# Kernel optimization log

Measured on AMD Instinct MI355X. Metric: run time of the kernel, lower is better.

## Reference

```python
import jax, jax.numpy as jnp
import numpy as np
import math

B, IN_CH, OUT_CH, STYLE, KS, DIL, L = 16, 128, 256, 512, 3, 1, 16384


def setup_inputs() -> dict:
    key = jax.random.key(0)
    ks = jax.random.split(key, 6)
    return {
        "x": jax.random.normal(ks[0], (B, IN_CH, L), jnp.float32),
        "style": jax.random.normal(ks[1], (B, STYLE), jnp.float32),
        "conv_weight": jax.random.normal(ks[2], (1, OUT_CH, IN_CH, KS), jnp.float32),
        "mod_weight": jax.random.normal(ks[3], (IN_CH, STYLE), jnp.float32),
        "mod_bias": jnp.ones((IN_CH,), jnp.float32),  # bias_init=1 in EqualLinear
        "out_v": jax.random.normal(ks[4], (IN_CH, OUT_CH // 2, 1), jnp.float32),
        "out_g": jax.random.uniform(ks[5], (IN_CH, 1, 1), jnp.float32, 0.5, 1.5),
        "out_bias": jnp.zeros((IN_CH,), jnp.float32),
    }


def reference(x, style, conv_weight, mod_weight, mod_bias, out_v, out_g, out_bias):
    scale_conv = 1.0 / math.sqrt(IN_CH * KS ** 2)  # fan_in = in_channel * k**2
    scale_mod = 1.0 / math.sqrt(STYLE)             # EqualLinear scale, lr_mul=1

    # modulation: EqualLinear(style_dim -> in_channel)
    s = style @ (mod_weight * scale_mod).T + mod_bias            # [B, I]

    # per-sample modulated + demodulated conv weight
    w = scale_conv * conv_weight * s[:, None, :, None]           # [B, O, I, K]
    demod = jax.lax.rsqrt(jnp.sum(w * w, axis=(2, 3)) + 1e-8)    # [B, O]
    w = w * demod[:, :, None, None]

    # grouped (groups=batch) dilated conv1d == per-sample conv via unfold + einsum
    pad = (KS - 1) // 2 * DIL
    xp = jnp.pad(x, ((0, 0), (0, 0), (pad, pad)))
    patches = jnp.stack([xp[:, :, k * DIL:k * DIL + L] for k in range(KS)], axis=2)  # [B, I, K, L]
    out = jnp.einsum('boik,bikl->bol', w, patches)               # [B, O, L]

    # gated tanh-sigmoid
    xa, xb = jnp.split(out, 2, axis=1)
    g = jnp.tanh(xa) * jax.nn.sigmoid(xb)                        # [B, O//2, L]

    # weight-normed 1x1 conv (dim=0: norm over in_ch and k per out channel)
    vnorm = jnp.sqrt(jnp.sum(out_v * out_v, axis=(1, 2), keepdims=True))
    w1 = (out_g * out_v / vnorm)[:, :, 0]                        # [R, O//2]
    y = jnp.einsum('oc,bcl->bol', w1, g) + out_bias[None, :, None]

    return (y + x) * math.sqrt(0.5)
```

## Files before the change

### kernel.cpp

```cpp
#include <hip/hip_runtime.h>
#include <hip/hip_bf16.h>
#include <math.h>

typedef float f32x4 __attribute__((ext_vector_type(4)));
typedef short bh8  __attribute__((ext_vector_type(8)));
typedef unsigned int u32x4 __attribute__((ext_vector_type(4)));

#define B_   16
#define IC   128
#define OC   256
#define RC   128
#define STY  512
#define KS_  3
#define LL   16384
#define LT   128

#define WS_S_OFF   0
#define WS_W_OFF   8192
#define WS_W1_OFF  (8192 + 3145728)

#define SMEM_BYTES 33792

__device__ __forceinline__ unsigned short f2b(float f) {
    union { float f; unsigned int u; } z; z.f = f;
    unsigned int u = z.u;
    return (unsigned short)((u + 0x7fffu + ((u >> 16) & 1u)) >> 16);
}

__device__ __forceinline__ float b2f(unsigned int u16) {
    union { unsigned int u; float f; } z; z.u = u16 << 16;
    return z.f;
}

__device__ __forceinline__ unsigned int pack2bf(float a, float b) {
    __hip_bfloat162 p = __float22bfloat162_rn(make_float2(a, b));
    return *(unsigned int*)&p;
}

__global__ void k_style(const float* __restrict__ style, const float* __restrict__ mw,
                        const float* __restrict__ mb, float* __restrict__ s_out) {
    const int b = blockIdx.x, i = threadIdx.x;
    const float4* st = (const float4*)(style + b * STY);
    const float4* w  = (const float4*)(mw + (size_t)i * STY);
    float acc = 0.f;
#pragma unroll 4
    for (int j = 0; j < STY / 4; ++j) {
        float4 a = st[j], c = w[j];
        acc += a.x * c.x + a.y * c.y + a.z * c.z + a.w * c.w;
    }
    s_out[b * IC + i] = acc * 0.044194173824159216f + mb[i];
}

__global__ void k_modw(const float* __restrict__ cw, const float* __restrict__ s,
                       unsigned short* __restrict__ wbf) {
    const int o = blockIdx.x, b = blockIdx.y, i = threadIdx.x;
    const float sv = s[b * IC + i] * 0.029462782549439476f;
    const float w0 = cw[(o * IC + i) * KS_ + 0] * sv;
    const float w1 = cw[(o * IC + i) * KS_ + 1] * sv;
    const float w2 = cw[(o * IC + i) * KS_ + 2] * sv;
    float ss = w0 * w0 + w1 * w1 + w2 * w2;
    for (int off = 32; off; off >>= 1) ss += __shfl_down(ss, off, 64);
    __shared__ float red[2];
    if ((i & 63) == 0) red[i >> 6] = ss;
    __syncthreads();
    const float d = rsqrtf(red[0] + red[1] + 1e-8f);
    unsigned short* dst = wbf + ((size_t)b * OC + o) * 384 + i;
    dst[0]   = f2b(w0 * d);
    dst[128] = f2b(w1 * d);
    dst[256] = f2b(w2 * d);
}

__global__ void k_w1(const float* __restrict__ v, const float* __restrict__ g,
                     unsigned short* __restrict__ w1bf) {
    const int o = blockIdx.x, c = threadIdx.x;
    const float vv = v[o * RC + c];
    float ss = vv * vv;
    for (int off = 32; off; off >>= 1) ss += __shfl_down(ss, off, 64);
    __shared__ float red[2];
    if ((c & 63) == 0) red[c >> 6] = ss;
    __syncthreads();
    w1bf[o * RC + c] = f2b(g[o] * vv * rsqrtf(red[0] + red[1]));
}

__global__ __launch_bounds__(512, 4) void k_main(
    const float* __restrict__ x, const unsigned short* __restrict__ wbf,
    const unsigned short* __restrict__ w1bf, const float* __restrict__ obias,
    float* __restrict__ out) {
    __shared__ alignas(16) char smem[SMEM_BYTES];

    const int t = threadIdx.x;
    const int lane = t & 63, wv = t >> 6;
    const int lm = lane & 15, kg = lane >> 4;
    const int c0 = wv * 16 + kg * 4;

    const int lid = blockIdx.y * (LL / LT) + blockIdx.x;
    const int swz = (lid & 7) * 256 + (lid >> 3);
    const int b  = swz >> 7;
    const int l0 = (swz & 127) * LT;

    const float* xb = x + (size_t)b * IC * LL + l0;

    {
        const int chb = wv * 16;
#pragma unroll
        for (int p = 0; p < 2; ++p) {
            const int pos = lane + p * 64;
            const int row = pos + 1;
#pragma unroll
            for (int h = 0; h < 2; ++h) {
                float xv[8];
#pragma unroll
                for (int c = 0; c < 8; ++c)
                    xv[c] = xb[(size_t)(chb + h * 8 + c) * LL + pos];
                u32x4 wvec;
                wvec.x = pack2bf(xv[0], xv[1]);
                wvec.y = pack2bf(xv[2], xv[3]);
                wvec.z = pack2bf(xv[4], xv[5]);
                wvec.w = pack2bf(xv[6], xv[7]);
                *(u32x4*)(smem + row * 256 +
                          (((chb + h * 8) * 2) ^ ((row & 15) << 4))) = wvec;
            }
        }
    }
    if (t < 128) {
        const float* hx = x + ((size_t)b * IC + t) * LL;
        float lf = (l0 > 0) ? hx[l0 - 1] : 0.f;
        float rt = (l0 + LT < LL) ? hx[l0 + LT] : 0.f;
        *(unsigned short*)(smem + 0 * 256 + ((t * 2) ^ ((0 & 15) << 4)))   = f2b(lf);
        *(unsigned short*)(smem + 129 * 256 + ((t * 2) ^ ((129 & 15) << 4))) = f2b(rt);
    }
    __syncthreads();

    f32x4 acc[2][8];
#pragma unroll
    for (int m = 0; m < 2; ++m)
#pragma unroll
        for (int nt = 0; nt < 8; ++nt) acc[m][nt] = (f32x4){0.f, 0.f, 0.f, 0.f};

    const unsigned short* wa = wbf + ((size_t)b * OC + wv * 16 + lm) * 384 + kg * 8;
    const unsigned short* wb2 = wa + 128 * 384;

    bh8 ca0 = *(const bh8*)(wa + 0);
    bh8 ca1 = *(const bh8*)(wb2 + 0);
#pragma unroll
    for (int kc = 0; kc < 12; ++kc) {
        bh8 na0 = ca0, na1 = ca1;
        if (kc < 11) {
            const int nkoff = ((kc + 1) >> 2) * 128 + ((kc + 1) & 3) * 32;
            na0 = *(const bh8*)(wa + nkoff);
            na1 = *(const bh8*)(wb2 + nkoff);
        }
        const int tap = kc >> 2;
        const int icb = (kc & 3) * 32;
#pragma unroll
        for (int nt = 0; nt < 8; ++nt) {
            const int lr = nt * 16 + lm + tap;
            const bh8 bf = *(const bh8*)(smem + lr * 256 +
                                         (((icb + kg * 8) * 2) ^ ((lr & 15) << 4)));
            acc[0][nt] = __builtin_amdgcn_mfma_f32_16x16x32_bf16(ca0, bf, acc[0][nt], 0, 0, 0);
            acc[1][nt] = __builtin_amdgcn_mfma_f32_16x16x32_bf16(ca1, bf, acc[1][nt], 0, 0, 0);
        }
        ca0 = na0; ca1 = na1;
    }

    unsigned long long xr[8];
#pragma unroll
    for (int nt = 0; nt < 8; ++nt) {
        const int row = nt * 16 + lm + 1;
        xr[nt] = *(const unsigned long long*)(smem + row * 256 +
                                             ((c0 * 2) ^ ((row & 15) << 4)));
    }

    const unsigned short* w1p = w1bf + (wv * 16 + lm) * RC + kg * 8;
    bh8 w1f[4];
#pragma unroll
    for (int kc = 0; kc < 4; ++kc) w1f[kc] = *(const bh8*)(w1p + kc * 32);

    unsigned long long gw[8];
#pragma unroll
    for (int nt = 0; nt < 8; ++nt) {
        float g4[4];
#pragma unroll
        for (int j = 0; j < 4; ++j) {
            const float xa = acc[0][nt][j], xg = acc[1][nt][j];
            const float th = 1.f - 2.f * __builtin_amdgcn_rcpf(__expf(2.f * xa) + 1.f);
            const float sg = __builtin_amdgcn_rcpf(1.f + __expf(-xg));
            g4[j] = th * sg;
        }
        gw[nt] = (unsigned long long)pack2bf(g4[0], g4[1]) |
                 ((unsigned long long)pack2bf(g4[2], g4[3]) << 32);
    }
    __syncthreads();

#pragma unroll
    for (int nt = 0; nt < 8; ++nt) {
        const int n = nt * 16 + lm;
        *(unsigned long long*)(smem + n * 256 + ((c0 * 2) ^ ((n & 15) << 4))) = gw[nt];
    }
    __syncthreads();

    f32x4 acc2[8];
#pragma unroll
    for (int nt = 0; nt < 8; ++nt) acc2[nt] = (f32x4){0.f, 0.f, 0.f, 0.f};
#pragma unroll
    for (int kc = 0; kc < 4; ++kc) {
#pragma unroll
        for (int nt = 0; nt < 8; ++nt) {
            const int n = nt * 16 + lm;
            const bh8 bf = *(const bh8*)(smem + n * 256 +
                                         (((kc * 32 + kg * 8) * 2) ^ ((n & 15) << 4)));
            acc2[nt] = __builtin_amdgcn_mfma_f32_16x16x32_bf16(w1f[kc], bf, acc2[nt], 0, 0, 0);
        }
    }
    __syncthreads();

    const float4 bias4 = *(const float4*)(obias + c0);
    const float bias[4] = {bias4.x, bias4.y, bias4.z, bias4.w};
#pragma unroll
    for (int nt = 0; nt < 8; ++nt) {
        const int n = nt * 16 + lm;
        float o4[4];
#pragma unroll
        for (int j = 0; j < 4; ++j)
            o4[j] = (acc2[nt][j] + bias[j] + b2f((unsigned int)(xr[nt] >> (16 * j)) & 0xffffu))
                    * 0.70710678118654752f;
        *(unsigned long long*)(smem + n * 264 + c0 * 2) =
            (unsigned long long)pack2bf(o4[0], o4[1]) |
            ((unsigned long long)pack2bf(o4[2], o4[3]) << 32);
    }
    __syncthreads();

    {
        const int p4 = t & 31;
        const int cb = t >> 5;
        float* ob = out + (size_t)b * IC * LL + l0 + p4 * 4;
#pragma unroll
        for (int h = 0; h < 2; ++h) {
            const int chb = cb * 4 + h * 64;
            unsigned long long yq[4];
#pragma unroll
            for (int q = 0; q < 4; ++q)
                yq[q] = *(const unsigned long long*)(smem + (p4 * 4 + q) * 264 + chb * 2);
#pragma unroll
            for (int e = 0; e < 4; ++e) {
                float4 ov;
                ov.x = b2f((unsigned int)(yq[0] >> (16 * e)) & 0xffffu);
                ov.y = b2f((unsigned int)(yq[1] >> (16 * e)) & 0xffffu);
                ov.z = b2f((unsigned int)(yq[2] >> (16 * e)) & 0xffffu);
                ov.w = b2f((unsigned int)(yq[3] >> (16 * e)) & 0xffffu);
                *(float4*)(ob + (size_t)(chb + e) * LL) = ov;
            }
        }
    }
}

extern "C" void kernel_launch(void* const* d_in, const int* in_sizes, int n_in,
                              void* d_out, int out_size, void* d_ws, size_t ws_size,
                              hipStream_t stream) {
    (void)in_sizes; (void)n_in; (void)out_size; (void)ws_size;
    const float* x        = (const float*)d_in[0];
    const float* style    = (const float*)d_in[1];
    const float* conv_w   = (const float*)d_in[2];
    const float* mod_w    = (const float*)d_in[3];
    const float* mod_b    = (const float*)d_in[4];
    const float* out_v    = (const float*)d_in[5];
    const float* out_g    = (const float*)d_in[6];
    const float* out_bias = (const float*)d_in[7];
    float* out = (float*)d_out;

    float* s_buf = (float*)((char*)d_ws + WS_S_OFF);
    unsigned short* wbf  = (unsigned short*)((char*)d_ws + WS_W_OFF);
    unsigned short* w1bf = (unsigned short*)((char*)d_ws + WS_W1_OFF);

    k_style<<<dim3(B_), 128, 0, stream>>>(style, mod_w, mod_b, s_buf);
    k_modw<<<dim3(OC, B_), 128, 0, stream>>>(conv_w, s_buf, wbf);
    k_w1<<<dim3(RC), 128, 0, stream>>>(out_v, out_g, w1bf);
    k_main<<<dim3(LL / LT, B_), 512, 0, stream>>>(x, wbf, w1bf, out_bias, out);
}
```

Measured before the change: 143.0 us.

## Process two L-tiles per block with register prefetch of the next x tile

Each block now handles two consecutive 128-position tiles. The x data for the second tile is loaded into registers while the first tile's conv and gate stages run, which hides global load latency. The grid is halved to a 1D launch with an XCD-aware batch mapping. This adds 32+ registers per thread, which could reduce occupancy under the 512x4 launch bounds or cause spills.

New measurement: 306.7 us. 2.14x slower.

```diff
diff --git a/kernel.cpp b/kernel.cpp
--- a/kernel.cpp
+++ b/kernel.cpp
@@ -14,6 +14,7 @@
 #define KS_  3
 #define LL   16384
 #define LT   128
+#define NT_  2
 
 #define WS_S_OFF   0
 #define WS_W_OFF   8192
@@ -93,162 +94,223 @@
     const int lm = lane & 15, kg = lane >> 4;
     const int c0 = wv * 16 + kg * 4;
 
-    const int lid = blockIdx.y * (LL / LT) + blockIdx.x;
-    const int swz = (lid & 7) * 256 + (lid >> 3);
-    const int b  = swz >> 7;
-    const int l0 = (swz & 127) * LT;
-
-    const float* xb = x + (size_t)b * IC * LL + l0;
-
-    {
-        const int chb = wv * 16;
-#pragma unroll
-        for (int p = 0; p < 2; ++p) {
-            const int pos = lane + p * 64;
-            const int row = pos + 1;
-#pragma unroll
-            for (int h = 0; h < 2; ++h) {
-                float xv[8];
+    const int lid = blockIdx.x;
+    const int xcd = lid & 7, idx = lid >> 3;
+    const int b   = xcd * 2 + (idx >> 6);
+    const int l0b = (idx & 63) * (LT * NT_);
+
+    const float* xbase = x + (size_t)b * IC * LL;
+    const unsigned short* wa  = wbf + ((size_t)b * OC + wv * 16 + lm) * 384 + kg * 8;
+    const unsigned short* wb2 = wa + 128 * 384;
+    const unsigned short* w1p = w1bf + (wv * 16 + lm) * RC + kg * 8;
+
+    float pf0[16], pf1[16];
+    float pfh0 = 0.f, pfh1 = 0.f;
+
+#pragma unroll
+    for (int tt = 0; tt < NT_; ++tt) {
+        const int l0 = l0b + tt * LT;
+        const float* xb = xbase + l0;
+
+        if (tt == 1) __syncthreads();
+
+        if (tt == 0) {
+            const int chb = wv * 16;
+#pragma unroll
+            for (int p = 0; p < 2; ++p) {
+                const int pos = lane + p * 64;
+                const int row = pos + 1;
+#pragma unroll
+                for (int h = 0; h < 2; ++h) {
+                    float xv[8];
+#pragma unroll
+                    for (int c = 0; c < 8; ++c)
+                        xv[c] = xb[(size_t)(chb + h * 8 + c) * LL + pos];
+                    u32x4 wvec;
+                    wvec.x = pack2bf(xv[0], xv[1]);
+                    wvec.y = pack2bf(xv[2], xv[3]);
+                    wvec.z = pack2bf(xv[4], xv[5]);
+                    wvec.w = pack2bf(xv[6], xv[7]);
+                    *(u32x4*)(smem + row * 256 +
+                              (((chb + h * 8) * 2) ^ ((row & 15) << 4))) = wvec;
+                }
+            }
+            if (t < 128) {
+                const float* hx = xbase + (size_t)t * LL;
+                float lf = (l0 > 0) ? hx[l0 - 1] : 0.f;
+                float rt = (l0 + LT < LL) ? hx[l0 + LT] : 0.f;
+                *(unsigned short*)(smem + 0 * 256 + ((t * 2) ^ ((0 & 15) << 4)))     = f2b(lf);
+                *(unsigned short*)(smem + 129 * 256 + ((t * 2) ^ ((129 & 15) << 4))) = f2b(rt);
+            }
+        } else {
+            const int chb = wv * 16;
+#pragma unroll
+            for (int p = 0; p < 2; ++p) {
+                const int row = lane + p * 64 + 1;
+#pragma unroll
+                for (int h = 0; h < 2; ++h) {
+                    u32x4 wvec;
+                    if (h == 0) {
+                        wvec.x = pack2bf(pf0[p * 8 + 0], pf0[p * 8 + 1]);
+                        wvec.y = pack2bf(pf0[p * 8 + 2], pf0[p * 8 + 3]);
+                        wvec.z = pack2bf(pf0[p * 8 + 4], pf0[p * 8 + 5]);
+                        wvec.w = pack2bf(pf0[p * 8 + 6], pf0[p * 8 + 7]);
+                    } else {
+                        wvec.x = pack2bf(pf1[p * 8 + 0], pf1[p * 8 + 1]);
+                        wvec.y = pack2bf(pf1[p * 8 + 2], pf1[p * 8 + 3]);
+                        wvec.z = pack2bf(pf1[p * 8 + 4], pf1[p * 8 + 5]);
+                        wvec.w = pack2bf(pf1[p * 8 + 6], pf1[p * 8 + 7]);
+                    }
+                    *(u32x4*)(smem + row * 256 +
+                              (((chb + h * 8) * 2) ^ ((row & 15) << 4))) = wvec;
+                }
+            }
+            if (t < 128) {
+                *(unsigned short*)(smem + 0 * 256 + ((t * 2) ^ ((0 & 15) << 4)))     = f2b(pfh0);
+                *(unsigned short*)(smem + 129 * 256 + ((t * 2) ^ ((129 & 15) << 4))) = f2b(pfh1);
+            }
+        }
+        __syncthreads();
+
+        if (tt == 0) {
+            const float* xb1 = xbase + l0b + LT;
+#pragma unroll
+            for (int p = 0; p < 2; ++p)
 #pragma unroll
                 for (int c = 0; c < 8; ++c)
-                    xv[c] = xb[(size_t)(chb + h * 8 + c) * LL + pos];
-                u32x4 wvec;
-                wvec.x = pack2bf(xv[0], xv[1]);
-                wvec.y = pack2bf(xv[2], xv[3]);
-                wvec.z = pack2bf(xv[4], xv[5]);
-                wvec.w = pack2bf(xv[6], xv[7]);
-                *(u32x4*)(smem + row * 256 +
-                          (((chb + h * 8) * 2) ^ ((row & 15) << 4))) = wvec;
-            }
-        }
-    }
-    if (t < 128) {
-        const float* hx = x + ((size_t)b * IC + t) * LL;
-        float lf = (l0 > 0) ? hx[l0 - 1] : 0.f;
-        float rt = (l0 + LT < LL) ? hx[l0 + LT] : 0.f;
-        *(unsigned short*)(smem + 0 * 256 + ((t * 2) ^ ((0 & 15) << 4)))   = f2b(lf);
-        *(unsigned short*)(smem + 129 * 256 + ((t * 2) ^ ((129 & 15) << 4))) = f2b(rt);
-    }
-    __syncthreads();
-
-    f32x4 acc[2][8];
-#pragma unroll
-    for (int m = 0; m < 2; ++m)
-#pragma unroll
-        for (int nt = 0; nt < 8; ++nt) acc[m][nt] = (f32x4){0.f, 0.f, 0.f, 0.f};
-
-    const unsigned short* wa = wbf + ((size_t)b * OC + wv * 16 + lm) * 384 + kg * 8;
-    const unsigned short* wb2 = wa + 128 * 384;
-
-    bh8 ca0 = *(const bh8*)(wa + 0);
-    bh8 ca1 = *(const bh8*)(wb2 + 0);
-#pragma unroll
-    for (int kc = 0; kc < 12; ++kc) {
-        bh8 na0 = ca0, na1 = ca1;
-        if (kc < 11) {
-            const int nkoff = ((kc + 1) >> 2) * 128 + ((kc + 1) & 3) * 32;
-            na0 = *(const bh8*)(wa + nkoff);
-            na1 = *(const bh8*)(wb2 + nkoff);
-        }
-        const int tap = kc >> 2;
-        const int icb = (kc & 3) * 32;
+                    pf0[p * 8 + c] = xb1[(size_t)(wv * 16 + c) * LL + lane + p * 64];
+            if (t < 128) {
+                const float* hx = xbase + (size_t)t * LL;
+                pfh0 = hx[l0b + LT - 1];
+                pfh1 = (l0b + 2 * LT < LL) ? hx[l0b + 2 * LT] : 0.f;
+            }
+        }
+
+        f32x4 acc[2][8];
+#pragma unroll
+        for (int m = 0; m < 2; ++m)
+#pragma unroll
+            for (int nt = 0; nt < 8; ++nt) acc[m][nt] = (f32x4){0.f, 0.f, 0.f, 0.f};
+
+        bh8 ca0 = *(const bh8*)(wa + 0);
+        bh8 ca1 = *(const bh8*)(wb2 + 0);
+#pragma unroll
+        for (int kc = 0; kc < 12; ++kc) {
+            bh8 na0 = ca0, na1 = ca1;
+            if (kc < 11) {
+                const int nkoff = ((kc + 1) >> 2) * 128 + ((kc + 1) & 3) * 32;
+                na0 = *(const bh8*)(wa + nkoff);
+                na1 = *(const bh8*)(wb2 + nkoff);
+            }
+            const int tap = kc >> 2;
+            const int icb = (kc & 3) * 32;
+#pragma unroll
+            for (int nt = 0; nt < 8; ++nt) {
+                const int lr = nt * 16 + lm + tap;
+                const bh8 bf = *(const bh8*)(smem + lr * 256 +
+                                             (((icb + kg * 8) * 2) ^ ((lr & 15) << 4)));
+                acc[0][nt] = __builtin_amdgcn_mfma_f32_16x16x32_bf16(ca0, bf, acc[0][nt], 0, 0, 0);
+                acc[1][nt] = __builtin_amdgcn_mfma_f32_16x16x32_bf16(ca1, bf, acc[1][nt], 0, 0, 0);
+            }
+            ca0 = na0; ca1 = na1;
+        }
+
+        unsigned long long xr[8];
 #pragma unroll
         for (int nt = 0; nt < 8; ++nt) {
-            const int lr = nt * 16 + lm + tap;
-            const bh8 bf = *(const bh8*)(smem + lr * 256 +
-                                         (((icb + kg * 8) * 2) ^ ((lr & 15) << 4)));
-            acc[0][nt] = __builtin_amdgcn_mfma_f32_16x16x32_bf16(ca0, bf, acc[0][nt], 0, 0, 0);
-            acc[1][nt] = __builtin_amdgcn_mfma_f32_16x16x32_bf16(ca1, bf, acc[1][nt], 0, 0, 0);
-        }
-        ca0 = na0; ca1 = na1;
-    }
-
-    unsigned long long xr[8];
-#pragma unroll
-    for (int nt = 0; nt < 8; ++nt) {
-        const int row = nt * 16 + lm + 1;
-        xr[nt] = *(const unsigned long long*)(smem + row * 256 +
-                                             ((c0 * 2) ^ ((row & 15) << 4)));
-    }
-
-    const unsigned short* w1p = w1bf + (wv * 16 + lm) * RC + kg * 8;
-    bh8 w1f[4];
-#pragma unroll
-    for (int kc = 0; kc < 4; ++kc) w1f[kc] = *(const bh8*)(w1p + kc * 32);
-
-    unsigned long long gw[8];
-#pragma unroll
-    for (int nt = 0; nt < 8; ++nt) {
-        float g4[4];
-#pragma unroll
-        for (int j = 0; j < 4; ++j) {
-            const float xa = acc[0][nt][j], xg = acc[1][nt][j];
-            const float th = 1.f - 2.f * __builtin_amdgcn_rcpf(__expf(2.f * xa) + 1.f);
-            const float sg = __builtin_amdgcn_rcpf(1.f + __expf(-xg));
-            g4[j] = th * sg;
-        }
-        gw[nt] = (unsigned long long)pack2bf(g4[0], g4[1]) |
-                 ((unsigned long long)pack2bf(g4[2], g4[3]) << 32);
-    }
-    __syncthreads();
-
-#pragma unroll
-    for (int nt = 0; nt < 8; ++nt) {
-        const int n = nt * 16 + lm;
-        *(unsigned long long*)(smem + n * 256 + ((c0 * 2) ^ ((n & 15) << 4))) = gw[nt];
-    }
-    __syncthreads();
-
-    f32x4 acc2[8];
-#pragma unroll
-    for (int nt = 0; nt < 8; ++nt) acc2[nt] = (f32x4){0.f, 0.f, 0.f, 0.f};
-#pragma unroll
-    for (int kc = 0; kc < 4; ++kc) {
+            const int row = nt * 16 + lm + 1;
+            xr[nt] = *(const unsigned long long*)(smem + row * 256 +
+                                                 ((c0 * 2) ^ ((row & 15) << 4)));
+        }
+
+        bh8 w1f[4];
+#pragma unroll
+        for (int kc = 0; kc < 4; ++kc) w1f[kc] = *(const bh8*)(w1p + kc * 32);
+
+        unsigned long long gw[8];
+#pragma unroll
+        for (int nt = 0; nt < 8; ++nt) {
+            float g4[4];
+#pragma unroll
+            for (int j = 0; j < 4; ++j) {
+                const float xa = acc[0][nt][j], xg = acc[1][nt][j];
+                const float th = 1.f - 2.f * __builtin_amdgcn_rcpf(__expf(2.f * xa) + 1.f);
+                const float sg = __builtin_amdgcn_rcpf(1.f + __expf(-xg));
+                g4[j] = th * sg;
+            }
+            gw[nt] = (unsigned long long)pack2bf(g4[0], g4[1]) |
+                     ((unsigned long long)pack2bf(g4[2], g4[3]) << 32);
+        }
+        __syncthreads();
+
 #pragma unroll
         for (int nt = 0; nt < 8; ++nt) {
             const int n = nt * 16 + lm;
-            const bh8 bf = *(const bh8*)(smem + n * 256 +
-                                         (((kc * 32 + kg * 8) * 2) ^ ((n & 15) << 4)));
-            acc2[nt] = __builtin_amdgcn_mfma_f32_16x16x32_bf16(w1f[kc], bf, acc2[nt], 0, 0, 0);
-        }
-    }
-    __syncthreads();
-
-    const float4 bias4 = *(const float4*)(obias + c0);
-    const float bias[4] = {bias4.x, bias4.y, bias4.z, bias4.w};
-#pragma unroll
-    for (int nt = 0; nt < 8; ++nt) {
-        const int n = nt * 16 + lm;
-        float o4[4];
-#pragma unroll
-        for (int j = 0; j < 4; ++j)
-            o4[j] = (acc2[nt][j] + bias[j] + b2f((unsigned int)(xr[nt] >> (16 * j)) & 0xffffu))
-                    * 0.70710678118654752f;
-        *(unsigned long long*)(smem + n * 264 + c0 * 2) =
-            (unsigned long long)pack2bf(o4[0], o4[1]) |
-            ((unsigned long long)pack2bf(o4[2], o4[3]) << 32);
-    }
-    __syncthreads();
-
-    {
-        const int p4 = t & 31;
-        const int cb = t >> 5;
-        float* ob = out + (size_t)b * IC * LL + l0 + p4 * 4;
-#pragma unroll
-        for (int h = 0; h < 2; ++h) {
-            const int chb = cb * 4 + h * 64;
-            unsigned long long yq[4];
-#pragma unroll
-            for (int q = 0; q < 4; ++q)
-                yq[q] = *(const unsigned long long*)(smem + (p4 * 4 + q) * 264 + chb * 2);
-#pragma unroll
-            for (int e = 0; e < 4; ++e) {
-                float4 ov;
-                ov.x = b2f((unsigned int)(yq[0] >> (16 * e)) & 0xffffu);
-                ov.y = b2f((unsigned int)(yq[1] >> (16 * e)) & 0xffffu);
-                ov.z = b2f((unsigned int)(yq[2] >> (16 * e)) & 0xffffu);
-                ov.w = b2f((unsigned int)(yq[3] >> (16 * e)) & 0xffffu);
-                *(float4*)(ob + (size_t)(chb + e) * LL) = ov;
+            *(unsigned long long*)(smem + n * 256 + ((c0 * 2) ^ ((n & 15) << 4))) = gw[nt];
+        }
+
+        if (tt == 0) {
+            const float* xb1 = xbase + l0b + LT;
+#pragma unroll
+            for (int p = 0; p < 2; ++p)
+#pragma unroll
+                for (int c = 0; c < 8; ++c)
+                    pf1[p * 8 + c] = xb1[(size_t)(wv * 16 + 8 + c) * LL + lane + p * 64];
+        }
+        __syncthreads();
+
+        f32x4 acc2[8];
+#pragma unroll
+        for (int nt = 0; nt < 8; ++nt) acc2[nt] = (f32x4){0.f, 0.f, 0.f, 0.f};
+#pragma unroll
+        for (int kc = 0; kc < 4; ++kc) {
+#pragma unroll
+            for (int nt = 0; nt < 8; ++nt) {
+                const int n = nt * 16 + lm;
+                const bh8 bf = *(const bh8*)(smem + n * 256 +
+                                             (((kc * 32 + kg * 8) * 2) ^ ((n & 15) << 4)));
+                acc2[nt] = __builtin_amdgcn_mfma_f32_16x16x32_bf16(w1f[kc], bf, acc2[nt], 0, 0, 0);
+            }
+        }
+        __syncthreads();
+
+        const float4 bias4 = *(const float4*)(obias + c0);
+        const float bias[4] = {bias4.x, bias4.y, bias4.z, bias4.w};
+#pragma unroll
+        for (int nt = 0; nt < 8; ++nt) {
+            const int n = nt * 16 + lm;
+            float o4[4];
+#pragma unroll
+            for (int j = 0; j < 4; ++j)
+                o4[j] = (acc2[nt][j] + bias[j] +
+                         b2f((unsigned int)(xr[nt] >> (16 * j)) & 0xffffu))
+                        * 0.70710678118654752f;
+            *(unsigned long long*)(smem + n * 264 + c0 * 2) =
+                (unsigned long long)pack2bf(o4[0], o4[1]) |
+                ((unsigned long long)pack2bf(o4[2], o4[3]) << 32);
+        }
+        __syncthreads();
+
+        {
+            const int p4 = t & 31;
+            const int cb = t >> 5;
+            float* ob = out + (size_t)b * IC * LL + l0 + p4 * 4;
+#pragma unroll
+            for (int h = 0; h < 2; ++h) {
+                const int chb = cb * 4 + h * 64;
+                unsigned long long yq[4];
+#pragma unroll
+                for (int q = 0; q < 4; ++q)
+                    yq[q] = *(const unsigned long long*)(smem + (p4 * 4 + q) * 264 + chb * 2);
+#pragma unroll
+                for (int e = 0; e < 4; ++e) {
+                    float4 ov;
+                    ov.x = b2f((unsigned int)(yq[0] >> (16 * e)) & 0xffffu);
+                    ov.y = b2f((unsigned int)(yq[1] >> (16 * e)) & 0xffffu);
+                    ov.z = b2f((unsigned int)(yq[2] >> (16 * e)) & 0xffffu);
+                    ov.w = b2f((unsigned int)(yq[3] >> (16 * e)) & 0xffffu);
+                    *(float4*)(ob + (size_t)(chb + e) * LL) = ov;
+                }
             }
         }
     }
@@ -275,5 +337,5 @@
     k_style<<<dim3(B_), 128, 0, stream>>>(style, mod_w, mod_b, s_buf);
     k_modw<<<dim3(OC, B_), 128, 0, stream>>>(conv_w, s_buf, wbf);
     k_w1<<<dim3(RC), 128, 0, stream>>>(out_v, out_g, w1bf);
-    k_main<<<dim3(LL / LT, B_), 512, 0, stream>>>(x, wbf, w1bf, out_bias, out);
-}
+    k_main<<<dim3(B_ * LL / (LT * NT_)), 512, 0, stream>>>(x, wbf, w1bf, out_bias, out);
+}
```

## Transpose second MFMA to write output directly and fold residual into accumulator

Applied to the files above, without the earlier changes.

The 1x1 output conv MFMA now runs with operands swapped, so each lane holds four consecutive positions of a single output channel and stores float4 straight to global memory. This removes the LDS staging transpose, two barriers, and the bf16 round-trip of the output. The residual, bias and sqrt(0.5) scale are preloaded as the accumulator's initial value, with the scale folded into w1 at preparation time. The grid also becomes one-dimensional. The trade-off is 16-byte stores strided across channels (64B contiguous per row segment), which may coalesce less well than the previous layout.

Result: faster. 123.9 us (-13.3%).

```diff
diff --git a/kernel.cpp b/kernel.cpp
--- a/kernel.cpp
+++ b/kernel.cpp
@@ -19,7 +19,7 @@
 #define WS_W_OFF   8192
 #define WS_W1_OFF  (8192 + 3145728)
 
-#define SMEM_BYTES 33792
+#define SMEM_BYTES 33280
 
 __device__ __forceinline__ unsigned short f2b(float f) {
     union { float f; unsigned int u; } z; z.f = f;
@@ -79,7 +79,7 @@
     __shared__ float red[2];
     if ((c & 63) == 0) red[c >> 6] = ss;
     __syncthreads();
-    w1bf[o * RC + c] = f2b(g[o] * vv * rsqrtf(red[0] + red[1]));
+    w1bf[o * RC + c] = f2b(g[o] * vv * rsqrtf(red[0] + red[1]) * 0.70710678118654752f);
 }
 
 __global__ __launch_bounds__(512, 4) void k_main(
@@ -93,7 +93,7 @@
     const int lm = lane & 15, kg = lane >> 4;
     const int c0 = wv * 16 + kg * 4;
 
-    const int lid = blockIdx.y * (LL / LT) + blockIdx.x;
+    const int lid = blockIdx.x;
     const int swz = (lid & 7) * 256 + (lid >> 3);
     const int b  = swz >> 7;
     const int l0 = (swz & 127) * LT;
@@ -126,7 +126,7 @@
         const float* hx = x + ((size_t)b * IC + t) * LL;
         float lf = (l0 > 0) ? hx[l0 - 1] : 0.f;
         float rt = (l0 + LT < LL) ? hx[l0 + LT] : 0.f;
-        *(unsigned short*)(smem + 0 * 256 + ((t * 2) ^ ((0 & 15) << 4)))   = f2b(lf);
+        *(unsigned short*)(smem + 0 * 256 + ((t * 2) ^ ((0 & 15) << 4)))     = f2b(lf);
         *(unsigned short*)(smem + 129 * 256 + ((t * 2) ^ ((129 & 15) << 4))) = f2b(rt);
     }
     __syncthreads();
@@ -163,15 +163,21 @@
         ca0 = na0; ca1 = na1;
     }
 
-    unsigned long long xr[8];
-#pragma unroll
-    for (int nt = 0; nt < 8; ++nt) {
-        const int row = nt * 16 + lm + 1;
-        xr[nt] = *(const unsigned long long*)(smem + row * 256 +
-                                             ((c0 * 2) ^ ((row & 15) << 4)));
-    }
-
-    const unsigned short* w1p = w1bf + (wv * 16 + lm) * RC + kg * 8;
+    const int myc = wv * 16 + lm;
+    const float bias = obias[myc];
+    f32x4 cin[8];
+#pragma unroll
+    for (int m = 0; m < 8; ++m) {
+#pragma unroll
+        for (int j = 0; j < 4; ++j) {
+            const int row = m * 16 + kg * 4 + j + 1;
+            const unsigned short xu = *(const unsigned short*)(
+                smem + row * 256 + ((myc * 2) ^ ((row & 15) << 4)));
+            cin[m][j] = (b2f(xu) + bias) * 0.70710678118654752f;
+        }
+    }
+
+    const unsigned short* w1p = w1bf + (size_t)myc * RC + kg * 8;
     bh8 w1f[4];
 #pragma unroll
     for (int kc = 0; kc < 4; ++kc) w1f[kc] = *(const bh8*)(w1p + kc * 32);
@@ -199,58 +205,20 @@
     }
     __syncthreads();
 
-    f32x4 acc2[8];
-#pragma unroll
-    for (int nt = 0; nt < 8; ++nt) acc2[nt] = (f32x4){0.f, 0.f, 0.f, 0.f};
-#pragma unroll
-    for (int kc = 0; kc < 4; ++kc) {
-#pragma unroll
-        for (int nt = 0; nt < 8; ++nt) {
-            const int n = nt * 16 + lm;
-            const bh8 bf = *(const bh8*)(smem + n * 256 +
+    float* orow = out + ((size_t)b * IC + myc) * LL + l0 + kg * 4;
+#pragma unroll
+    for (int m = 0; m < 8; ++m) {
+        f32x4 acc2 = cin[m];
+#pragma unroll
+        for (int kc = 0; kc < 4; ++kc) {
+            const int n = m * 16 + lm;
+            const bh8 ga = *(const bh8*)(smem + n * 256 +
                                          (((kc * 32 + kg * 8) * 2) ^ ((n & 15) << 4)));
-            acc2[nt] = __builtin_amdgcn_mfma_f32_16x16x32_bf16(w1f[kc], bf, acc2[nt], 0, 0, 0);
-        }
-    }
-    __syncthreads();
-
-    const float4 bias4 = *(const float4*)(obias + c0);
-    const float bias[4] = {bias4.x, bias4.y, bias4.z, bias4.w};
-#pragma unroll
-    for (int nt = 0; nt < 8; ++nt) {
-        const int n = nt * 16 + lm;
-        float o4[4];
-#pragma unroll
-        for (int j = 0; j < 4; ++j)
-            o4[j] = (acc2[nt][j] + bias[j] + b2f((unsigned int)(xr[nt] >> (16 * j)) & 0xffffu))
-                    * 0.70710678118654752f;
-        *(unsigned long long*)(smem + n * 264 + c0 * 2) =
-            (unsigned long long)pack2bf(o4[0], o4[1]) |
-            ((unsigned long long)pack2bf(o4[2], o4[3]) << 32);
-    }
-    __syncthreads();
-
-    {
-        const int p4 = t & 31;
-        const int cb = t >> 5;
-        float* ob = out + (size_t)b * IC * LL + l0 + p4 * 4;
-#pragma unroll
-        for (int h = 0; h < 2; ++h) {
-            const int chb = cb * 4 + h * 64;
-            unsigned long long yq[4];
-#pragma unroll
-            for (int q = 0; q < 4; ++q)
-                yq[q] = *(const unsigned long long*)(smem + (p4 * 4 + q) * 264 + chb * 2);
-#pragma unroll
-            for (int e = 0; e < 4; ++e) {
-                float4 ov;
-                ov.x = b2f((unsigned int)(yq[0] >> (16 * e)) & 0xffffu);
-                ov.y = b2f((unsigned int)(yq[1] >> (16 * e)) & 0xffffu);
-                ov.z = b2f((unsigned int)(yq[2] >> (16 * e)) & 0xffffu);
-                ov.w = b2f((unsigned int)(yq[3] >> (16 * e)) & 0xffffu);
-                *(float4*)(ob + (size_t)(chb + e) * LL) = ov;
-            }
-        }
+            acc2 = __builtin_amdgcn_mfma_f32_16x16x32_bf16(ga, w1f[kc], acc2, 0, 0, 0);
+        }
+        float4 ov;
+        ov.x = acc2[0]; ov.y = acc2[1]; ov.z = acc2[2]; ov.w = acc2[3];
+        *(float4*)(orow + m * 16) = ov;
     }
 }
 
@@ -275,5 +243,5 @@
     k_style<<<dim3(B_), 128, 0, stream>>>(style, mod_w, mod_b, s_buf);
     k_modw<<<dim3(OC, B_), 128, 0, stream>>>(conv_w, s_buf, wbf);
     k_w1<<<dim3(RC), 128, 0, stream>>>(out_v, out_g, w1bf);
-    k_main<<<dim3(LL / LT, B_), 512, 0, stream>>>(x, wbf, w1bf, out_bias, out);
-}
+    k_main<<<dim3(B_ * LL / LT), 512, 0, stream>>>(x, wbf, w1bf, out_bias, out);
+}
```
